# Kernel tuning notes

Hardware: AMD Instinct MI355X
Metric: run time of the kernel (lower is better)

## Reference

```python
import jax, jax.numpy as jnp
import numpy as np

EPS = 1e-5

def _ln(x, g, b):
    mu = jnp.mean(x, axis=-1, keepdims=True)
    var = jnp.mean(jnp.square(x - mu), axis=-1, keepdims=True)
    return (x - mu) * jax.lax.rsqrt(var + EPS) * g + b


def setup_inputs() -> dict:
    key = jax.random.key(0)
    ks = jax.random.split(key, 16)
    B, T, D, H = 8, 4096, 512, 1024
    s_d = 1.0 / np.sqrt(D)
    s_h = 1.0 / np.sqrt(H)
    return {
        "x": jax.random.normal(ks[0], (B, T, D), dtype=jnp.float32),
        "gamma": jnp.ones((D,), jnp.float32),
        "beta": jnp.zeros((D,), jnp.float32),
        "Wq": jax.random.uniform(ks[1], (D, H), jnp.float32, -s_d, s_d),
        "bq": jax.random.uniform(ks[2], (H,), jnp.float32, -s_d, s_d),
        "Wk": jax.random.uniform(ks[3], (D, H), jnp.float32, -s_d, s_d),
        "bk": jax.random.uniform(ks[4], (H,), jnp.float32, -s_d, s_d),
        "Wv": jax.random.uniform(ks[5], (D, H), jnp.float32, -s_d, s_d),
        "bv": jax.random.uniform(ks[6], (H,), jnp.float32, -s_d, s_d),
        "wbias": jax.random.uniform(ks[7], (H,), jnp.float32, 0.0, 1.0),
        "Wo": jax.random.uniform(ks[8], (H, D), jnp.float32, -s_h, s_h),
        "bo": jax.random.uniform(ks[9], (D,), jnp.float32, -s_h, s_h),
        "W1": jax.random.uniform(ks[10], (D, H), jnp.float32, -s_d, s_d),
        "b1": jax.random.uniform(ks[11], (H,), jnp.float32, -s_d, s_d),
        "W2": jax.random.uniform(ks[12], (H, D), jnp.float32, -s_h, s_h),
        "b2": jax.random.uniform(ks[13], (D,), jnp.float32, -s_h, s_h),
    }


def reference(x, gamma, beta, Wq, bq, Wk, bk, Wv, bv, wbias, Wo, bo, W1, b1, W2, b2):
    # --- pre-LN ---
    x1 = _ln(x, gamma, beta)                      # [B,T,D]
    # --- AFTFull attention (NOTE: sums over BATCH dim 0, as in original repo) ---
    Q = jnp.einsum('btd,dh->bth', x1, Wq) + bq    # [B,T,H]
    K = jnp.einsum('btd,dh->bth', x1, Wk) + bk
    V = jnp.einsum('btd,dh->bth', x1, Wv) + bv
    Q_sig = jax.nn.sigmoid(Q)
    numer = jnp.exp(K + wbias)                    # [B,T,H]
    denom = jnp.sum(numer, axis=0)                # [T,H]
    weighted = jnp.sum(numer * V, axis=0) / denom # [T,H]
    Yt = Q_sig * weighted                         # [B,T,H] (broadcast)
    Yt = jnp.einsum('bth,hd->btd', Yt, Wo) + bo   # [B,T,D]
    x2 = Yt + x1                                  # residual (dropout = identity, eval)
    # --- second LN (same params, as in original) + MLP ---
    x3 = _ln(x2, gamma, beta)
    h = jax.nn.gelu(jnp.einsum('btd,dh->bth', x3, W1) + b1, approximate=False)
    m = jnp.einsum('bth,hd->btd', h, W2) + b2
    # original: out = dropout(m) + m  ==  2*m at eval (no residual to x2)
    return m + m
```

## Files before the change

kernel.cpp:

```cpp
#include <hip/hip_runtime.h>
#include <hip/hip_bf16.h>
#include <cstdint>

using u16 = unsigned short;
using u32 = unsigned int;

typedef __bf16 bf16x8 __attribute__((ext_vector_type(8)));
typedef float  f32x4  __attribute__((ext_vector_type(4)));

#define DEV static __device__ __forceinline__

DEV float bf2f(u16 u){ union { u32 u; float f; } c; c.u = ((u32)u) << 16; return c.f; }

DEV u16 f2bf(float f){
  __bf16 h = (__bf16)f;
  return __builtin_bit_cast(u16, h);
}

DEV float fast_rcp(float x){ return __builtin_amdgcn_rcpf(x); }

DEV void async16(const u16* g, u16* l){
  __builtin_amdgcn_global_load_lds((const __attribute__((address_space(1))) u32*)g,
                                   (__attribute__((address_space(3))) u32*)l,
                                   16, 0, 0);
}

#define BARRIER() __builtin_amdgcn_s_barrier()
#define LGKM0() do { __asm__ volatile("s_waitcnt lgkmcnt(0)" ::: "memory"); \
                     __builtin_amdgcn_sched_barrier(0); } while (0)
#define VMCNT(n) __asm__ volatile("s_waitcnt vmcnt(" #n ")" ::: "memory")

__global__ __launch_bounds__(256)
void transpose_all(const float* __restrict__ W0, const float* __restrict__ W1,
                   const float* __restrict__ W2, const float* __restrict__ W3,
                   const float* __restrict__ W4, const float* __restrict__ W5,
                   u16* __restrict__ T0, u16* __restrict__ T1, u16* __restrict__ T2,
                   u16* __restrict__ T3, u16* __restrict__ T4, u16* __restrict__ T5){
  const int z = blockIdx.z;
  const float* W; u16* WT; int R, C;
  switch (z){
    case 0:  W = W0; WT = T0; R = 512;  C = 1024; break;
    case 1:  W = W1; WT = T1; R = 512;  C = 1024; break;
    case 2:  W = W2; WT = T2; R = 512;  C = 1024; break;
    case 3:  W = W3; WT = T3; R = 1024; C = 512;  break;
    case 4:  W = W4; WT = T4; R = 512;  C = 1024; break;
    default: W = W5; WT = T5; R = 1024; C = 512;  break;
  }
  const int c0 = blockIdx.x * 32, r0 = blockIdx.y * 32;
  if (c0 >= C || r0 >= R) return;
  __shared__ float tile[32][33];
  const int tx = threadIdx.x, ty = threadIdx.y;
  #pragma unroll
  for (int j = 0; j < 4; ++j)
    tile[ty + j*8][tx] = W[(size_t)(r0 + ty + j*8) * C + (c0 + tx)];
  __syncthreads();
  #pragma unroll
  for (int j = 0; j < 4; ++j)
    WT[(size_t)(c0 + ty + j*8) * R + (r0 + tx)] = f2bf(tile[tx][ty + j*8]);
}

template<bool BF16IN>
__global__ __launch_bounds__(256)
void ln_kernel(const void* __restrict__ xin, const float* __restrict__ gamma,
               const float* __restrict__ beta, u16* __restrict__ xout){
  const int wid = threadIdx.x >> 6;
  const int lane = threadIdx.x & 63;
  const size_t row = (size_t)blockIdx.x * 4 + wid;
  const int d0 = lane * 8;
  float v[8];
  if constexpr (BF16IN){
    const u16* xp = (const u16*)xin + row * 512 + d0;
    uint4 p = *(const uint4*)xp;
    const u16* s = (const u16*)&p;
    #pragma unroll
    for (int i = 0; i < 8; ++i) v[i] = bf2f(s[i]);
  } else {
    const float* xp = (const float*)xin + row * 512 + d0;
    float4 p0 = *(const float4*)xp;
    float4 p1 = *(const float4*)(xp + 4);
    v[0]=p0.x; v[1]=p0.y; v[2]=p0.z; v[3]=p0.w;
    v[4]=p1.x; v[5]=p1.y; v[6]=p1.z; v[7]=p1.w;
  }
  float s = 0.f, sq = 0.f;
  #pragma unroll
  for (int i = 0; i < 8; ++i){ s += v[i]; sq += v[i]*v[i]; }
  #pragma unroll
  for (int o = 32; o >= 1; o >>= 1){ s += __shfl_xor(s, o); sq += __shfl_xor(sq, o); }
  const float mu  = s * (1.0f/512.0f);
  const float var = sq * (1.0f/512.0f) - mu*mu;
  const float rstd = rsqrtf(var + 1e-5f);
  const float4 g0 = *(const float4*)(gamma + d0);
  const float4 g1 = *(const float4*)(gamma + d0 + 4);
  const float4 b0 = *(const float4*)(beta + d0);
  const float4 b1 = *(const float4*)(beta + d0 + 4);
  float gg[8] = {g0.x,g0.y,g0.z,g0.w,g1.x,g1.y,g1.z,g1.w};
  float bb[8] = {b0.x,b0.y,b0.z,b0.w,b1.x,b1.y,b1.z,b1.w};
  u16 o8[8];
  #pragma unroll
  for (int i = 0; i < 8; ++i)
    o8[i] = f2bf((v[i]-mu)*rstd*gg[i] + bb[i]);
  *(uint4*)(xout + row*512 + d0) = *(const uint4*)o8;
}

__global__ __launch_bounds__(256)
void aft_fused(const u16* __restrict__ numer, const u16* __restrict__ V,
               const u16* __restrict__ qs, u16* __restrict__ yt){
  const size_t TH = (size_t)4096 * 1024;
  const size_t i8 = ((size_t)blockIdx.x * 256 + threadIdx.x) * 8;
  float den[8], ws[8];
  #pragma unroll
  for (int j = 0; j < 8; ++j){ den[j] = 0.f; ws[j] = 0.f; }
  #pragma unroll
  for (int b = 0; b < 8; ++b){
    uint4 pn = *(const uint4*)(numer + b*TH + i8);
    uint4 pv = *(const uint4*)(V     + b*TH + i8);
    const u16* n = (const u16*)&pn;
    const u16* v = (const u16*)&pv;
    #pragma unroll
    for (int j = 0; j < 8; ++j){ float nf = bf2f(n[j]); den[j] += nf; ws[j] += nf * bf2f(v[j]); }
  }
  float w[8];
  #pragma unroll
  for (int j = 0; j < 8; ++j) w[j] = ws[j] * fast_rcp(den[j]);
  #pragma unroll
  for (int b = 0; b < 8; ++b){
    uint4 pq = *(const uint4*)(qs + b*TH + i8);
    const u16* q = (const u16*)&pq;
    u16 o[8];
    #pragma unroll
    for (int j = 0; j < 8; ++j) o[j] = f2bf(bf2f(q[j]) * w[j]);
    *(uint4*)(yt + b*TH + i8) = *(const uint4*)o;
  }
}

template<int EPI, int KC>
__global__ __launch_bounds__(512, 2)
void gemm256(const u16* __restrict__ A, const u16* __restrict__ Bt,
             const float* __restrict__ bias0, const float* __restrict__ wbias,
             u16* __restrict__ out0, u16* __restrict__ out1, u16* __restrict__ out2,
             const float* __restrict__ bias1, const float* __restrict__ bias2,
             const u16* __restrict__ resid, float* __restrict__ outf){
  constexpr int NK = KC / 64;
  __shared__ __align__(16) char smem[65536];

  const int tid  = threadIdx.x;
  const int wid  = tid >> 6;
  const int lane = tid & 63;
  const int quad = lane >> 4;
  const int lr   = lane & 15;
  const int wm   = wid & 1;
  const int wn   = wid >> 1;

  const int nwg = gridDim.x;
  const int wg  = (blockIdx.x & 7) * (nwg >> 3) + (blockIdx.x >> 3);
  const int nNT = nwg >> 7;
  const int sgs = nNT << 2;
  const int sg  = wg / sgs;
  const int r   = wg - sg * sgs;
  const int tileM = (sg*4 + (r & 3)) * 256;
  const int tileN = (r >> 2) * 256;

  const u16* sA[2][2]; const u16* sB[2][2];
  {
    const int off0 = wid*1024 + lane*16;
    #pragma unroll
    for (int rr_ = 0; rr_ < 2; ++rr_){
      const int off = rr_*8192 + off0;
      const int rr  = off >> 7;
      const int g   = (((off >> 4) & 7) ^ (rr & 7)) * 8;
      #pragma unroll
      for (int h = 0; h < 2; ++h){
        sA[h][rr_] = A  + (size_t)(tileM + (rr>>6)*128 + h*64 + (rr&63)) * KC + g;
        sB[h][rr_] = Bt + (size_t)(tileN + (rr>>5)*64  + h*32 + (rr&31)) * KC + g;
      }
    }
  }
  auto stA = [&](int h, int kt){
    char* d = smem + h*16384 + wid*1024;
    async16(sA[h][0] + kt, (u16*)d);
    async16(sA[h][1] + kt, (u16*)(d + 8192));
  };
  auto stB = [&](int h, int kt){
    char* d = smem + 32768 + h*16384 + wid*1024;
    async16(sB[h][0] + kt, (u16*)d);
    async16(sB[h][1] + kt, (u16*)(d + 8192));
  };

  const int cO0  = ((quad)     ^ (lr & 7)) * 16;
  const int cO1  = ((quad ^ 4) ^ (lr & 7)) * 16;
  const int aRow = (wm*64 + lr) * 128;
  const int bRow = (wn*32 + lr) * 128;

  bf16x8 ar[4][2], br0[2][2], br1[2][2];
  f32x4 acc[2][2][4][2] = {};

  auto ldA = [&](int mh){
    #pragma unroll
    for (int i = 0; i < 4; ++i){
      ar[i][0] = *(const bf16x8*)(smem + mh*16384 + aRow + i*2048 + cO0);
      ar[i][1] = *(const bf16x8*)(smem + mh*16384 + aRow + i*2048 + cO1);
    }
  };
  auto ldB = [&](int nh, bf16x8 (&br)[2][2]){
    #pragma unroll
    for (int j = 0; j < 2; ++j){
      br[j][0] = *(const bf16x8*)(smem + 32768 + nh*16384 + bRow + j*2048 + cO0);
      br[j][1] = *(const bf16x8*)(smem + 32768 + nh*16384 + bRow + j*2048 + cO1);
    }
  };
  auto MF = [&](int mh, int nh, bf16x8 (&br)[2][2]){
    __builtin_amdgcn_s_setprio(1);
    #pragma unroll
    for (int i = 0; i < 4; ++i)
      #pragma unroll
      for (int j = 0; j < 2; ++j){
        acc[mh][nh][i][j] = __builtin_amdgcn_mfma_f32_16x16x32_bf16(br[j][0], ar[i][0], acc[mh][nh][i][j], 0, 0, 0);
        acc[mh][nh][i][j] = __builtin_amdgcn_mfma_f32_16x16x32_bf16(br[j][1], ar[i][1], acc[mh][nh][i][j], 0, 0, 0);
      }
    __builtin_amdgcn_s_setprio(0);
  };

  stA(0, 0); stB(0, 0); stB(1, 0); stA(1, 0);
  VMCNT(4);
  BARRIER();

  #pragma unroll 1
  for (int t = 0; t < NK-1; ++t){
    const int kt = (t+1)*64;
    ldA(0); ldB(0, br0);
    BARRIER(); LGKM0();
    MF(0, 0, br0);
    VMCNT(2);
    BARRIER();
    ldB(1, br1);
    stA(0, kt); stB(0, kt);
    BARRIER(); LGKM0();
    MF(0, 1, br1);
    VMCNT(4);
    BARRIER();
    ldA(1);
    stB(1, kt);
    BARRIER(); LGKM0();
    MF(1, 1, br1);
    BARRIER();
    stA(1, kt);
    MF(1, 0, br0);
    VMCNT(4);
    BARRIER();
  }
  ldA(0); ldB(0, br0);
  BARRIER(); LGKM0();
  MF(0, 0, br0);
  VMCNT(2);
  BARRIER();
  ldB(1, br1);
  BARRIER(); LGKM0();
  MF(0, 1, br1);
  VMCNT(0);
  BARRIER();
  ldA(1);
  BARRIER(); LGKM0();
  MF(1, 1, br1);
  BARRIER();
  MF(1, 0, br0);

  if (EPI == 3){
    #pragma unroll
    for (int mh = 0; mh < 2; ++mh)
    #pragma unroll
    for (int i = 0; i < 4; ++i){
      const int row = tileM + wm*128 + mh*64 + i*16 + lr;
      #pragma unroll
      for (int nh = 0; nh < 2; ++nh)
      #pragma unroll
      for (int j = 0; j < 2; ++j){
        const int colb = tileN + wn*64 + nh*32 + j*16 + quad*4;
        const float4 bvv = *(const float4*)(bias0 + colb);
        float4 o;
        #pragma unroll
        for (int r_ = 0; r_ < 4; ++r_)
          ((float*)&o)[r_] = 2.0f * (acc[mh][nh][i][j][r_] + ((const float*)&bvv)[r_]);
        *(float4*)(outf + (size_t)row * 512 + colb) = o;
      }
    }
    return;
  }

  char* eb = smem + wid * 2304;
  const int mat = (EPI == 0) ? (tileN >> 10) : 0;
  const float* biasP = bias0;
  u16* outP = out0;
  int ldO = 1024, cb0 = tileN + wn*64;
  if (EPI == 0){
    biasP = (mat==0) ? bias0 : (mat==1) ? bias1 : bias2;
    outP  = (mat==0) ? out0  : (mat==1) ? out1  : out2;
    cb0   = (tileN & 1023) + wn*64;
  } else if (EPI == 1){
    ldO = 512;
  }

  #pragma unroll
  for (int mh = 0; mh < 2; ++mh)
  #pragma unroll
  for (int i = 0; i < 4; ++i){
    const int row = tileM + wm*128 + mh*64 + i*16 + lr;
    #pragma unroll
    for (int nh = 0; nh < 2; ++nh)
    #pragma unroll
    for (int j = 0; j < 2; ++j){
      const int cl = (nh*2 + j)*16 + quad*4;
      const float4 bvv = *(const float4*)(biasP + cb0 + cl);
      u16 o[4];
      if (EPI == 0){
        float4 wbv = {0,0,0,0};
        if (mat == 1) wbv = *(const float4*)(wbias + cb0 + cl);
        #pragma unroll
        for (int r_ = 0; r_ < 4; ++r_){
          float v = acc[mh][nh][i][j][r_] + ((const float*)&bvv)[r_];
          if (mat == 0)      v = fast_rcp(1.0f + __expf(-v));
          else if (mat == 1) v = __expf(v + ((const float*)&wbv)[r_]);
          o[r_] = f2bf(v);
        }
      } else if (EPI == 1){
        uint2 pr = *(const uint2*)(resid + (size_t)row * 512 + cb0 + cl);
        const u16* rp = (const u16*)&pr;
        #pragma unroll
        for (int r_ = 0; r_ < 4; ++r_)
          o[r_] = f2bf(acc[mh][nh][i][j][r_] + ((const float*)&bvv)[r_] + bf2f(rp[r_]));
      } else {
        #pragma unroll
        for (int r_ = 0; r_ < 4; ++r_){
          float v  = acc[mh][nh][i][j][r_] + ((const float*)&bvv)[r_];
          float u2 = 2.0f * v * (0.7978845608f + 0.0356774081f * v * v);
          float tg = 1.0f - 2.0f * fast_rcp(1.0f + __expf(u2));
          o[r_] = f2bf(0.5f * v * (1.0f + tg));
        }
      }
      *(uint2*)(eb + lr*144 + cl*2) = *(const uint2*)o;
    }
    __asm__ volatile("s_waitcnt lgkmcnt(0)" ::: "memory");
    uint4 p0 = *(const uint4*)(eb + lr*144 + quad*32);
    uint4 p1 = *(const uint4*)(eb + lr*144 + quad*32 + 16);
    __asm__ volatile("s_waitcnt lgkmcnt(0)" ::: "memory");
    u16* gp = outP + (size_t)row * ldO + cb0 + quad*16;
    *(uint4*)gp = p0;
    *(uint4*)(gp + 8) = p1;
  }
}

extern "C" void kernel_launch(void* const* d_in, const int* in_sizes, int n_in,
                              void* d_out, int out_size, void* d_ws, size_t ws_size,
                              hipStream_t stream) {
  const float* x     = (const float*)d_in[0];
  const float* gamma = (const float*)d_in[1];
  const float* beta  = (const float*)d_in[2];
  const float* Wq    = (const float*)d_in[3];
  const float* bq    = (const float*)d_in[4];
  const float* Wk    = (const float*)d_in[5];
  const float* bk    = (const float*)d_in[6];
  const float* Wv    = (const float*)d_in[7];
  const float* bv    = (const float*)d_in[8];
  const float* wbias = (const float*)d_in[9];
  const float* Wo    = (const float*)d_in[10];
  const float* bo    = (const float*)d_in[11];
  const float* W1    = (const float*)d_in[12];
  const float* b1    = (const float*)d_in[13];
  const float* W2    = (const float*)d_in[14];
  const float* b2    = (const float*)d_in[15];
  float* out = (float*)d_out;

  char* w = (char*)d_ws;
  const size_t MB = 1ull << 20;
  u16* WqkvT = (u16*)(w + 0*MB);
  u16* WoT   = (u16*)(w + 3*MB);
  u16* W1T   = (u16*)(w + 4*MB);
  u16* W2T   = (u16*)(w + 5*MB);
  u16* x1b   = (u16*)(w + 6*MB);
  u16* Qs    = (u16*)(w + 38*MB);
  u16* Nu    = (u16*)(w + 102*MB);
  u16* Vb    = (u16*)(w + 166*MB);
  u16* Yt    = Nu;
  u16* x2b   = Vb;
  u16* x3b   = (u16*)(w + 198*MB);
  u16* hb    = Qs;

  transpose_all<<<dim3(32, 32, 6), dim3(32, 8), 0, stream>>>(
      Wq, Wk, Wv, Wo, W1, W2,
      WqkvT, WqkvT + 1024*512, WqkvT + 2*1024*512, WoT, W1T, W2T);

  ln_kernel<false><<<8192, 256, 0, stream>>>(x, gamma, beta, x1b);

  gemm256<0, 512><<<1536, 512, 0, stream>>>(x1b, WqkvT,
      bq, wbias, Qs, Nu, Vb, bk, bv, nullptr, nullptr);

  aft_fused<<<2048, 256, 0, stream>>>(Nu, Vb, Qs, Yt);

  gemm256<1, 1024><<<256, 512, 0, stream>>>(Yt, WoT,
      bo, nullptr, x2b, nullptr, nullptr, nullptr, nullptr, x1b, nullptr);

  ln_kernel<true><<<8192, 256, 0, stream>>>(x2b, gamma, beta, x3b);

  gemm256<2, 512><<<512, 512, 0, stream>>>(x3b, W1T,
      b1, nullptr, hb, nullptr, nullptr, nullptr, nullptr, nullptr, nullptr);

  gemm256<3, 1024><<<256, 512, 0, stream>>>(hb, W2T,
      b2, nullptr, nullptr, nullptr, nullptr, nullptr, nullptr, nullptr, out);
}
```

Before: 455.9 us.

## Restructure GEMM main loop to double-buffered 32-wide K steps

```diff
diff --git a/kernel.cpp b/kernel.cpp
--- a/kernel.cpp
+++ b/kernel.cpp
@@ -25,7 +25,8 @@
                                    16, 0, 0);
 }
 
-#define BARRIER() __builtin_amdgcn_s_barrier()
+#define BARRIER() do { __builtin_amdgcn_s_barrier(); \
+                       __builtin_amdgcn_sched_barrier(0); } while (0)
 #define LGKM0() do { __asm__ volatile("s_waitcnt lgkmcnt(0)" ::: "memory"); \
                      __builtin_amdgcn_sched_barrier(0); } while (0)
 #define VMCNT(n) __asm__ volatile("s_waitcnt vmcnt(" #n ")" ::: "memory")
@@ -140,7 +141,7 @@
              u16* __restrict__ out0, u16* __restrict__ out1, u16* __restrict__ out2,
              const float* __restrict__ bias1, const float* __restrict__ bias2,
              const u16* __restrict__ resid, float* __restrict__ outf){
-  constexpr int NK = KC / 64;
+  constexpr int NKS = KC / 32;
   __shared__ __align__(16) char smem[65536];
 
   const int tid  = threadIdx.x;
@@ -160,109 +161,97 @@
   const int tileM = (sg*4 + (r & 3)) * 256;
   const int tileN = (r >> 2) * 256;
 
-  const u16* sA[2][2]; const u16* sB[2][2];
+  const u16 *pA0, *pA1, *pB0, *pB1;
   {
-    const int off0 = wid*1024 + lane*16;
-    #pragma unroll
-    for (int rr_ = 0; rr_ < 2; ++rr_){
-      const int off = rr_*8192 + off0;
-      const int rr  = off >> 7;
-      const int g   = (((off >> 4) & 7) ^ (rr & 7)) * 8;
+    const int o0 = tid << 4;
+    const int r0_ = o0 >> 6,          c0_ = (o0 >> 4) & 3;
+    const int r1_ = (o0 + 8192) >> 6, c1_ = c0_;
+    pA0 = A  + (size_t)(tileM + r0_) * KC + (c0_ ^ ((r0_ >> 1) & 3)) * 8;
+    pA1 = A  + (size_t)(tileM + r1_) * KC + (c1_ ^ ((r1_ >> 1) & 3)) * 8;
+    pB0 = Bt + (size_t)(tileN + r0_) * KC + (c0_ ^ ((r0_ >> 1) & 3)) * 8;
+    pB1 = Bt + (size_t)(tileN + r1_) * KC + (c1_ ^ ((r1_ >> 1) & 3)) * 8;
+  }
+  auto stageA = [&](char* nb, int kt){
+    char* d = nb + wid*1024 + (lane << 4);
+    async16(pA0 + kt, (u16*)d);
+    async16(pA1 + kt, (u16*)(d + 8192));
+  };
+  auto stageB = [&](char* nb, int kt){
+    char* d = nb + 16384 + wid*1024 + (lane << 4);
+    async16(pB0 + kt, (u16*)d);
+    async16(pB1 + kt, (u16*)(d + 8192));
+  };
+
+  int aOff[2][4], bOff[2][2];
+  #pragma unroll
+  for (int mh = 0; mh < 2; ++mh)
+    #pragma unroll
+    for (int i = 0; i < 4; ++i){
+      const int rw = wm*128 + mh*64 + i*16 + lr;
+      aOff[mh][i] = rw*64 + ((quad ^ ((rw >> 1) & 3)) << 4);
+    }
+  #pragma unroll
+  for (int nh = 0; nh < 2; ++nh)
+    #pragma unroll
+    for (int j = 0; j < 2; ++j){
+      const int rw = wn*64 + nh*32 + j*16 + lr;
+      bOff[nh][j] = 16384 + rw*64 + ((quad ^ ((rw >> 1) & 3)) << 4);
+    }
+
+  bf16x8 ar[4], br[2][2];
+  f32x4 acc[2][2][4][2] = {};
+
+  auto ldA = [&](const char* cb, int mh){
+    #pragma unroll
+    for (int i = 0; i < 4; ++i) ar[i] = *(const bf16x8*)(cb + aOff[mh][i]);
+  };
+  auto ldB = [&](const char* cb){
+    #pragma unroll
+    for (int nh = 0; nh < 2; ++nh)
       #pragma unroll
-      for (int h = 0; h < 2; ++h){
-        sA[h][rr_] = A  + (size_t)(tileM + (rr>>6)*128 + h*64 + (rr&63)) * KC + g;
-        sB[h][rr_] = Bt + (size_t)(tileN + (rr>>5)*64  + h*32 + (rr&31)) * KC + g;
-      }
-    }
-  }
-  auto stA = [&](int h, int kt){
-    char* d = smem + h*16384 + wid*1024;
-    async16(sA[h][0] + kt, (u16*)d);
-    async16(sA[h][1] + kt, (u16*)(d + 8192));
-  };
-  auto stB = [&](int h, int kt){
-    char* d = smem + 32768 + h*16384 + wid*1024;
-    async16(sB[h][0] + kt, (u16*)d);
-    async16(sB[h][1] + kt, (u16*)(d + 8192));
-  };
-
-  const int cO0  = ((quad)     ^ (lr & 7)) * 16;
-  const int cO1  = ((quad ^ 4) ^ (lr & 7)) * 16;
-  const int aRow = (wm*64 + lr) * 128;
-  const int bRow = (wn*32 + lr) * 128;
-
-  bf16x8 ar[4][2], br0[2][2], br1[2][2];
-  f32x4 acc[2][2][4][2] = {};
-
-  auto ldA = [&](int mh){
-    #pragma unroll
-    for (int i = 0; i < 4; ++i){
-      ar[i][0] = *(const bf16x8*)(smem + mh*16384 + aRow + i*2048 + cO0);
-      ar[i][1] = *(const bf16x8*)(smem + mh*16384 + aRow + i*2048 + cO1);
-    }
-  };
-  auto ldB = [&](int nh, bf16x8 (&br)[2][2]){
-    #pragma unroll
-    for (int j = 0; j < 2; ++j){
-      br[j][0] = *(const bf16x8*)(smem + 32768 + nh*16384 + bRow + j*2048 + cO0);
-      br[j][1] = *(const bf16x8*)(smem + 32768 + nh*16384 + bRow + j*2048 + cO1);
-    }
-  };
-  auto MF = [&](int mh, int nh, bf16x8 (&br)[2][2]){
+      for (int j = 0; j < 2; ++j) br[nh][j] = *(const bf16x8*)(cb + bOff[nh][j]);
+  };
+  auto MF = [&](int mh){
     __builtin_amdgcn_s_setprio(1);
     #pragma unroll
     for (int i = 0; i < 4; ++i)
       #pragma unroll
-      for (int j = 0; j < 2; ++j){
-        acc[mh][nh][i][j] = __builtin_amdgcn_mfma_f32_16x16x32_bf16(br[j][0], ar[i][0], acc[mh][nh][i][j], 0, 0, 0);
-        acc[mh][nh][i][j] = __builtin_amdgcn_mfma_f32_16x16x32_bf16(br[j][1], ar[i][1], acc[mh][nh][i][j], 0, 0, 0);
-      }
+      for (int nh = 0; nh < 2; ++nh)
+        #pragma unroll
+        for (int j = 0; j < 2; ++j)
+          acc[mh][nh][i][j] = __builtin_amdgcn_mfma_f32_16x16x32_bf16(br[nh][j], ar[i], acc[mh][nh][i][j], 0, 0, 0);
     __builtin_amdgcn_s_setprio(0);
   };
 
-  stA(0, 0); stB(0, 0); stB(1, 0); stA(1, 0);
-  VMCNT(4);
-  BARRIER();
-
-  #pragma unroll 1
-  for (int t = 0; t < NK-1; ++t){
-    const int kt = (t+1)*64;
-    ldA(0); ldB(0, br0);
-    BARRIER(); LGKM0();
-    MF(0, 0, br0);
-    VMCNT(2);
-    BARRIER();
-    ldB(1, br1);
-    stA(0, kt); stB(0, kt);
-    BARRIER(); LGKM0();
-    MF(0, 1, br1);
-    VMCNT(4);
-    BARRIER();
-    ldA(1);
-    stB(1, kt);
-    BARRIER(); LGKM0();
-    MF(1, 1, br1);
-    BARRIER();
-    stA(1, kt);
-    MF(1, 0, br0);
-    VMCNT(4);
-    BARRIER();
-  }
-  ldA(0); ldB(0, br0);
-  BARRIER(); LGKM0();
-  MF(0, 0, br0);
-  VMCNT(2);
-  BARRIER();
-  ldB(1, br1);
-  BARRIER(); LGKM0();
-  MF(0, 1, br1);
+  stageA(smem, 0); stageB(smem, 0);
   VMCNT(0);
   BARRIER();
-  ldA(1);
-  BARRIER(); LGKM0();
-  MF(1, 1, br1);
-  BARRIER();
-  MF(1, 0, br0);
+
+  #pragma unroll 1
+  for (int t = 0; t < NKS-1; ++t){
+    const char* cb = smem + (t & 1)*32768;
+    char* nb = smem + ((t & 1) ^ 1)*32768;
+    const int kt = (t + 1) << 5;
+    stageA(nb, kt);
+    ldA(cb, 0); ldB(cb);
+    LGKM0();
+    MF(0);
+    stageB(nb, kt);
+    ldA(cb, 1);
+    LGKM0();
+    MF(1);
+    VMCNT(0);
+    BARRIER();
+  }
+  {
+    const char* cb = smem + ((NKS-1) & 1)*32768;
+    ldA(cb, 0); ldB(cb);
+    LGKM0();
+    MF(0);
+    ldA(cb, 1);
+    LGKM0();
+    MF(1);
+  }
 
   if (EPI == 3){
     #pragma unroll
@@ -286,6 +275,7 @@
     return;
   }
 
+  BARRIER();
   char* eb = smem + wid * 2304;
   const int mat = (EPI == 0) ? (tileN >> 10) : 0;
   const float* biasP = bias0;
```

New measurement: 490.5 us. 7.6% more time.

## Fuse first LayerNorm into weight-transpose kernel and use 128-tile GEMM for QKV

Applied to the files above, without the earlier changes.

```diff
diff --git a/kernel.cpp b/kernel.cpp
--- a/kernel.cpp
+++ b/kernel.cpp
@@ -31,12 +31,46 @@
 #define VMCNT(n) __asm__ volatile("s_waitcnt vmcnt(" #n ")" ::: "memory")
 
 __global__ __launch_bounds__(256)
-void transpose_all(const float* __restrict__ W0, const float* __restrict__ W1,
-                   const float* __restrict__ W2, const float* __restrict__ W3,
-                   const float* __restrict__ W4, const float* __restrict__ W5,
-                   u16* __restrict__ T0, u16* __restrict__ T1, u16* __restrict__ T2,
-                   u16* __restrict__ T3, u16* __restrict__ T4, u16* __restrict__ T5){
+void prep_fused(const float* __restrict__ W0, const float* __restrict__ W1,
+                const float* __restrict__ W2, const float* __restrict__ W3,
+                const float* __restrict__ W4, const float* __restrict__ W5,
+                u16* __restrict__ T0, u16* __restrict__ T1, u16* __restrict__ T2,
+                u16* __restrict__ T3, u16* __restrict__ T4, u16* __restrict__ T5,
+                const float* __restrict__ x, const float* __restrict__ gamma,
+                const float* __restrict__ beta, u16* __restrict__ x1b){
   const int z = blockIdx.z;
+  if (z >= 6){
+    const int bid = (z - 6) * 1024 + blockIdx.y * 32 + blockIdx.x;
+    const int tid = threadIdx.y * 32 + threadIdx.x;
+    const int wid = tid >> 6;
+    const int lane = tid & 63;
+    const size_t row = (size_t)bid * 4 + wid;
+    const int d0 = lane * 8;
+    const float* xp = x + row * 512 + d0;
+    float4 p0 = *(const float4*)xp;
+    float4 p1 = *(const float4*)(xp + 4);
+    float v[8] = {p0.x,p0.y,p0.z,p0.w,p1.x,p1.y,p1.z,p1.w};
+    float s = 0.f, sq = 0.f;
+    #pragma unroll
+    for (int i = 0; i < 8; ++i){ s += v[i]; sq += v[i]*v[i]; }
+    #pragma unroll
+    for (int o = 32; o >= 1; o >>= 1){ s += __shfl_xor(s, o); sq += __shfl_xor(sq, o); }
+    const float mu  = s * (1.0f/512.0f);
+    const float var = sq * (1.0f/512.0f) - mu*mu;
+    const float rstd = rsqrtf(var + 1e-5f);
+    const float4 g0 = *(const float4*)(gamma + d0);
+    const float4 g1 = *(const float4*)(gamma + d0 + 4);
+    const float4 b0 = *(const float4*)(beta + d0);
+    const float4 b1 = *(const float4*)(beta + d0 + 4);
+    float gg[8] = {g0.x,g0.y,g0.z,g0.w,g1.x,g1.y,g1.z,g1.w};
+    float bb[8] = {b0.x,b0.y,b0.z,b0.w,b1.x,b1.y,b1.z,b1.w};
+    u16 o8[8];
+    #pragma unroll
+    for (int i = 0; i < 8; ++i)
+      o8[i] = f2bf((v[i]-mu)*rstd*gg[i] + bb[i]);
+    *(uint4*)(x1b + row*512 + d0) = *(const uint4*)o8;
+    return;
+  }
   const float* W; u16* WT; int R, C;
   switch (z){
     case 0:  W = W0; WT = T0; R = 512;  C = 1024; break;
@@ -130,6 +164,158 @@
     #pragma unroll
     for (int j = 0; j < 8; ++j) o[j] = f2bf(bf2f(q[j]) * w[j]);
     *(uint4*)(yt + b*TH + i8) = *(const uint4*)o;
+  }
+}
+
+template<int EPI, int KC>
+__global__ __launch_bounds__(256, 3)
+void gemm128(const u16* __restrict__ A, const u16* __restrict__ Bt, int nTiles,
+             const float* __restrict__ bias0, const float* __restrict__ wbias,
+             u16* __restrict__ out0, u16* __restrict__ out1, u16* __restrict__ out2,
+             const float* __restrict__ bias1, const float* __restrict__ bias2,
+             const u16* __restrict__ resid, float* __restrict__ outf){
+  __shared__ u16 ldsA[128*64];
+  __shared__ u16 ldsB[128*64];
+  const int tid  = threadIdx.x;
+  const int wid  = tid >> 6;
+  const int lane = tid & 63;
+  const int quad = lane >> 4;
+  const int lr   = lane & 15;
+
+  const int lin = blockIdx.x;
+  const int GS  = 16 * nTiles;
+  const int g   = lin / GS;
+  const int rem = lin - g * GS;
+  const int tileM = (g * 16 + (rem & 15)) * 128;
+  const int tileN = (rem >> 4) * 128;
+
+  const int wmBase = (wid & 1) * 64;
+  const int wnBase = (wid >> 1) * 64;
+
+  f32x4 acc[4][4] = {};
+
+  int srow[4], scb[4];
+  #pragma unroll
+  for (int r = 0; r < 4; ++r){
+    const int off = r*4096 + wid*1024 + lane*16;
+    srow[r] = off >> 7;
+    scb[r]  = ((off >> 4) & 7) ^ (srow[r] & 7);
+  }
+  const u16* aSrc[4]; const u16* bSrc[4];
+  #pragma unroll
+  for (int r = 0; r < 4; ++r){
+    aSrc[r] = A  + (size_t)(tileM + srow[r]) * KC + scb[r]*8;
+    bSrc[r] = Bt + (size_t)(tileN + srow[r]) * KC + scb[r]*8;
+  }
+
+  int aOff[2][4], bOff[2][4];
+  #pragma unroll
+  for (int s = 0; s < 2; ++s)
+    #pragma unroll
+    for (int i = 0; i < 4; ++i){
+      const int m = wmBase + i*16 + lr;
+      const int n = wnBase + i*16 + lr;
+      aOff[s][i] = m*128 + (((s*4 + quad) ^ (m & 7)) * 16);
+      bOff[s][i] = n*128 + (((s*4 + quad) ^ (n & 7)) * 16);
+    }
+
+  #pragma unroll
+  for (int kt = 0; kt < KC; kt += 64){
+    #pragma unroll
+    for (int r = 0; r < 4; ++r){
+      async16(aSrc[r] + kt, (u16*)((char*)ldsA + r*4096 + wid*1024));
+      async16(bSrc[r] + kt, (u16*)((char*)ldsB + r*4096 + wid*1024));
+    }
+    __syncthreads();
+    #pragma unroll
+    for (int s = 0; s < 2; ++s){
+      bf16x8 ar[4], br[4];
+      #pragma unroll
+      for (int i = 0; i < 4; ++i) ar[i] = *(const bf16x8*)((const char*)ldsA + aOff[s][i]);
+      #pragma unroll
+      for (int i = 0; i < 4; ++i) br[i] = *(const bf16x8*)((const char*)ldsB + bOff[s][i]);
+      #pragma unroll
+      for (int i = 0; i < 4; ++i)
+        #pragma unroll
+        for (int j = 0; j < 4; ++j)
+          acc[i][j] = __builtin_amdgcn_mfma_f32_16x16x32_bf16(br[j], ar[i], acc[i][j], 0, 0, 0);
+    }
+    __syncthreads();
+  }
+
+  if (EPI == 3){
+    #pragma unroll
+    for (int j = 0; j < 4; ++j){
+      const int colb = tileN + wnBase + j*16 + quad*4;
+      const float4 bvv = *(const float4*)(bias0 + colb);
+      #pragma unroll
+      for (int i = 0; i < 4; ++i){
+        const int row = tileM + wmBase + i*16 + lr;
+        float4 o;
+        #pragma unroll
+        for (int r = 0; r < 4; ++r)
+          ((float*)&o)[r] = 2.0f * (acc[i][j][r] + ((const float*)&bvv)[r]);
+        *(float4*)(outf + (size_t)row * 512 + colb) = o;
+      }
+    }
+    return;
+  }
+
+  u16* eb = ldsA + wid * 1152;
+  const int mat = (EPI == 0) ? (tileN >> 10) : 0;
+  const float* biasP = bias0;
+  u16* outP = out0;
+  int ldO = 1024, cb0 = tileN + wnBase;
+  if (EPI == 0){
+    biasP = (mat==0) ? bias0 : (mat==1) ? bias1 : bias2;
+    outP  = (mat==0) ? out0  : (mat==1) ? out1  : out2;
+    cb0   = (tileN & 1023) + wnBase;
+  } else if (EPI == 1){
+    ldO = 512;
+  }
+
+  #pragma unroll
+  for (int i = 0; i < 4; ++i){
+    const int row = tileM + wmBase + i*16 + lr;
+    #pragma unroll
+    for (int j = 0; j < 4; ++j){
+      const int cl = j*16 + quad*4;
+      const float4 bvv = *(const float4*)(biasP + cb0 + cl);
+      u16 o[4];
+      if (EPI == 0){
+        float4 wbv = {0,0,0,0};
+        if (mat == 1) wbv = *(const float4*)(wbias + cb0 + cl);
+        #pragma unroll
+        for (int r = 0; r < 4; ++r){
+          float v = acc[i][j][r] + ((const float*)&bvv)[r];
+          if (mat == 0)      v = fast_rcp(1.0f + __expf(-v));
+          else if (mat == 1) v = __expf(v + ((const float*)&wbv)[r]);
+          o[r] = f2bf(v);
+        }
+      } else if (EPI == 1){
+        uint2 pr = *(const uint2*)(resid + (size_t)row * 512 + cb0 + cl);
+        const u16* rp = (const u16*)&pr;
+        #pragma unroll
+        for (int r = 0; r < 4; ++r)
+          o[r] = f2bf(acc[i][j][r] + ((const float*)&bvv)[r] + bf2f(rp[r]));
+      } else {
+        #pragma unroll
+        for (int r = 0; r < 4; ++r){
+          float v = acc[i][j][r] + ((const float*)&bvv)[r];
+          float u2 = 2.0f * v * (0.7978845608f + 0.0356774081f * v * v);
+          float t  = 1.0f - 2.0f * fast_rcp(1.0f + __expf(u2));
+          o[r] = f2bf(0.5f * v * (1.0f + t));
+        }
+      }
+      *(uint2*)(eb + lr*72 + cl) = *(const uint2*)o;
+    }
+    __asm__ volatile("s_waitcnt lgkmcnt(0)" ::: "memory");
+    uint4 p0 = *(const uint4*)(eb + lr*72 + quad*16);
+    uint4 p1 = *(const uint4*)(eb + lr*72 + quad*16 + 8);
+    __asm__ volatile("s_waitcnt lgkmcnt(0)" ::: "memory");
+    u16* gp = outP + (size_t)row * ldO + cb0 + quad*16;
+    *(uint4*)gp = p0;
+    *(uint4*)(gp + 8) = p1;
   }
 }
 
@@ -287,17 +473,14 @@
   }
 
   char* eb = smem + wid * 2304;
-  const int mat = (EPI == 0) ? (tileN >> 10) : 0;
+  const int mat = 0;
   const float* biasP = bias0;
   u16* outP = out0;
   int ldO = 1024, cb0 = tileN + wn*64;
-  if (EPI == 0){
-    biasP = (mat==0) ? bias0 : (mat==1) ? bias1 : bias2;
-    outP  = (mat==0) ? out0  : (mat==1) ? out1  : out2;
-    cb0   = (tileN & 1023) + wn*64;
-  } else if (EPI == 1){
+  if (EPI == 1){
     ldO = 512;
   }
+  (void)mat;
 
   #pragma unroll
   for (int mh = 0; mh < 2; ++mh)
@@ -311,17 +494,7 @@
       const int cl = (nh*2 + j)*16 + quad*4;
       const float4 bvv = *(const float4*)(biasP + cb0 + cl);
       u16 o[4];
-      if (EPI == 0){
-        float4 wbv = {0,0,0,0};
-        if (mat == 1) wbv = *(const float4*)(wbias + cb0 + cl);
-        #pragma unroll
-        for (int r_ = 0; r_ < 4; ++r_){
-          float v = acc[mh][nh][i][j][r_] + ((const float*)&bvv)[r_];
-          if (mat == 0)      v = fast_rcp(1.0f + __expf(-v));
-          else if (mat == 1) v = __expf(v + ((const float*)&wbv)[r_]);
-          o[r_] = f2bf(v);
-        }
-      } else if (EPI == 1){
+      if (EPI == 1){
         uint2 pr = *(const uint2*)(resid + (size_t)row * 512 + cb0 + cl);
         const u16* rp = (const u16*)&pr;
         #pragma unroll
@@ -384,13 +557,12 @@
   u16* x3b   = (u16*)(w + 198*MB);
   u16* hb    = Qs;
 
-  transpose_all<<<dim3(32, 32, 6), dim3(32, 8), 0, stream>>>(
+  prep_fused<<<dim3(32, 32, 14), dim3(32, 8), 0, stream>>>(
       Wq, Wk, Wv, Wo, W1, W2,
-      WqkvT, WqkvT + 1024*512, WqkvT + 2*1024*512, WoT, W1T, W2T);
-
-  ln_kernel<false><<<8192, 256, 0, stream>>>(x, gamma, beta, x1b);
-
-  gemm256<0, 512><<<1536, 512, 0, stream>>>(x1b, WqkvT,
+      WqkvT, WqkvT + 1024*512, WqkvT + 2*1024*512, WoT, W1T, W2T,
+      x, gamma, beta, x1b);
+
+  gemm128<0, 512><<<256*24, 256, 0, stream>>>(x1b, WqkvT, 24,
       bq, wbias, Qs, Nu, Vb, bk, bv, nullptr, nullptr);
 
   aft_fused<<<2048, 256, 0, stream>>>(Nu, Vb, Qs, Yt);
```

New measurement: 480.6 us. 5.4% more time.
